# Optimization experiments

Hardware: AMD Instinct MI355X
Metric: run time of the kernel (lower is better)

The kernel has to match this reference:

```python
import jax, jax.numpy as jnp
import numpy as np

N_NODES = 100000


def setup_inputs() -> dict:
    key = jax.random.key(0)
    k1, k2, k3, k4, k5 = jax.random.split(key, 5)
    d_in, d_out, n_edges = 128, 128, 640000
    x = jax.random.normal(k1, (N_NODES, d_in), dtype=jnp.float32)
    edge_index = jax.random.randint(k2, (2, n_edges), 0, N_NODES, dtype=jnp.int64)
    # uniform(size, W) in the source is U(-1/sqrt(in), 1/sqrt(in)); scaled normal is fine as data
    s = 1.0 / np.sqrt(d_in)
    Wc = jax.random.normal(k3, (d_in, d_out), dtype=jnp.float32) * s
    Wn = jax.random.normal(k4, (d_in, d_out), dtype=jnp.float32) * s
    b = jax.random.normal(k5, (d_out,), dtype=jnp.float32) * s
    return {"x": x, "edge_index": edge_index, "Wc": Wc, "Wn": Wn, "b": b}


def reference(x, edge_index, Wc, Wn, b):
    row, col = edge_index[0], edge_index[1]
    alpha = x @ Wc                      # [N, out]
    beta = x @ Wn                       # [N, out]
    # Vectorized scatter-mean replacing the original per-node Python loop:
    # gamma[n] = mean(beta[col[row == n]])
    num = jax.ops.segment_sum(beta[col], row, num_segments=N_NODES)   # [N, out]
    cnt = jax.ops.segment_sum(jnp.ones_like(row, dtype=beta.dtype), row, num_segments=N_NODES)
    gamma = num / jnp.maximum(cnt, 1.0)[:, None]  # NOTE: unused below, exactly as in the original forward
    del gamma
    # The original returns alpha + beta + bias (gamma is dead code in the source).
    return alpha + beta + b
```

## Files before the change

### kernel.cpp

```cpp
#include <hip/hip_runtime.h>
#include <hip/hip_bf16.h>


#define NROWS 100000

typedef __attribute__((ext_vector_type(8))) __bf16 bf16x8;
typedef __attribute__((ext_vector_type(8))) unsigned short u16x8;
typedef __attribute__((ext_vector_type(4))) float f32x4;

__device__ __forceinline__ unsigned short f2bf(float f) {
    unsigned int u = __builtin_bit_cast(unsigned int, f);
    u += 0x7FFFu + ((u >> 16) & 1u);
    return (unsigned short)(u >> 16);
}

__device__ __forceinline__ bf16x8 pack8(const float4 lo, const float4 hi) {
    u16x8 r;
    r[0] = f2bf(lo.x); r[1] = f2bf(lo.y); r[2] = f2bf(lo.z); r[3] = f2bf(lo.w);
    r[4] = f2bf(hi.x); r[5] = f2bf(hi.y); r[6] = f2bf(hi.z); r[7] = f2bf(hi.w);
    return __builtin_bit_cast(bf16x8, r);
}

__global__ void prep_wt(const float* __restrict__ Wc, const float* __restrict__ Wn,
                        unsigned short* __restrict__ wt) {
    int i = blockIdx.x * 256 + threadIdx.x;
    int n = i >> 7, k = i & 127;
    wt[i] = f2bf(Wc[k * 128 + n] + Wn[k * 128 + n]);
}

__global__ __launch_bounds__(256) void gemm_bias(
    const float* __restrict__ x, const unsigned short* __restrict__ wt,
    const float* __restrict__ bias_g, float* __restrict__ out) {

    __shared__ __align__(16) unsigned short sWt[128 * 136];

    const int tid = threadIdx.x;
    #pragma unroll
    for (int it = 0; it < 8; ++it) {
        int idx8 = it * 256 + tid;
        int n = idx8 >> 4;
        int k = (idx8 & 15) << 3;
        *(u16x8*)&sWt[n * 136 + k] = *(const u16x8*)(wt + (idx8 << 3));
    }
    __syncthreads();

    const int wave = tid >> 6;
    const int lane = tid & 63;
    const int quad = lane >> 4;
    const int l16  = lane & 15;

    const long rowbase = (long)blockIdx.x * 128 + wave * 32;
    if (rowbase >= NROWS) return;

    float bv[8];
    #pragma unroll
    for (int ct = 0; ct < 8; ++ct) bv[ct] = bias_g[ct * 16 + l16];

    f32x4 acc[2][8] = {};

    const float* xr0 = x + (rowbase + l16) * 128;
    const float* xr1 = xr0 + 16 * 128;

    #pragma unroll
    for (int kc = 0; kc < 4; ++kc) {
        const int ko = kc * 32 + quad * 8;
        float4 a0lo = *(const float4*)(xr0 + ko);
        float4 a0hi = *(const float4*)(xr0 + ko + 4);
        float4 a1lo = *(const float4*)(xr1 + ko);
        float4 a1hi = *(const float4*)(xr1 + ko + 4);
        bf16x8 a0 = pack8(a0lo, a0hi);
        bf16x8 a1 = pack8(a1lo, a1hi);
        #pragma unroll
        for (int ct = 0; ct < 8; ++ct) {
            bf16x8 bf = *(const bf16x8*)&sWt[(ct * 16 + l16) * 136 + ko];
            acc[0][ct] = __builtin_amdgcn_mfma_f32_16x16x32_bf16(a0, bf, acc[0][ct], 0, 0, 0);
            acc[1][ct] = __builtin_amdgcn_mfma_f32_16x16x32_bf16(a1, bf, acc[1][ct], 0, 0, 0);
        }
    }

    #pragma unroll
    for (int mt = 0; mt < 2; ++mt) {
        #pragma unroll
        for (int r = 0; r < 4; ++r) {
            float* orow = out + (rowbase + mt * 16 + quad * 4 + r) * 128;
            #pragma unroll
            for (int ct = 0; ct < 8; ++ct) {
                orow[ct * 16 + l16] = acc[mt][ct][r] + bv[ct];
            }
        }
    }
}

extern "C" void kernel_launch(void* const* d_in, const int* in_sizes, int n_in,
                              void* d_out, int out_size, void* d_ws, size_t ws_size,
                              hipStream_t stream) {
    const float* x  = (const float*)d_in[0];
    const float* Wc = (const float*)d_in[2];
    const float* Wn = (const float*)d_in[3];
    const float* b  = (const float*)d_in[4];
    unsigned short* wt = (unsigned short*)d_ws;
    float* out = (float*)d_out;

    prep_wt<<<64, 256, 0, stream>>>(Wc, Wn, wt);
    const int nblocks = (NROWS + 127) / 128;
    gemm_bias<<<nblocks, 256, 0, stream>>>(x, wt, b, out);
}
```

Before: 112.9 us.

## Swap MFMA operands so each lane stores contiguous float4 outputs nontemporally

Swaps the A/B operands of the bf16 MFMA so the accumulator holds four consecutive output columns per lane instead of four rows. The epilogue can then write 16-byte vector stores with nontemporal hints instead of scalar 4-byte stores, and the bias is loaded as float4. It also replaces the manual round-to-nearest bf16 conversion with native __bf16 casts, which may lower to hardware convert instructions. The output is mathematically the same; the risk is small rounding-mode differences in the conversion.

```diff
diff --git a/kernel.cpp b/kernel.cpp
--- a/kernel.cpp
+++ b/kernel.cpp
@@ -8,31 +8,25 @@
 typedef __attribute__((ext_vector_type(8))) unsigned short u16x8;
 typedef __attribute__((ext_vector_type(4))) float f32x4;
 
-__device__ __forceinline__ unsigned short f2bf(float f) {
-    unsigned int u = __builtin_bit_cast(unsigned int, f);
-    u += 0x7FFFu + ((u >> 16) & 1u);
-    return (unsigned short)(u >> 16);
-}
-
 __device__ __forceinline__ bf16x8 pack8(const float4 lo, const float4 hi) {
-    u16x8 r;
-    r[0] = f2bf(lo.x); r[1] = f2bf(lo.y); r[2] = f2bf(lo.z); r[3] = f2bf(lo.w);
-    r[4] = f2bf(hi.x); r[5] = f2bf(hi.y); r[6] = f2bf(hi.z); r[7] = f2bf(hi.w);
-    return __builtin_bit_cast(bf16x8, r);
+    bf16x8 r;
+    r[0] = (__bf16)lo.x; r[1] = (__bf16)lo.y; r[2] = (__bf16)lo.z; r[3] = (__bf16)lo.w;
+    r[4] = (__bf16)hi.x; r[5] = (__bf16)hi.y; r[6] = (__bf16)hi.z; r[7] = (__bf16)hi.w;
+    return r;
 }
 
 __global__ void prep_wt(const float* __restrict__ Wc, const float* __restrict__ Wn,
-                        unsigned short* __restrict__ wt) {
+                        __bf16* __restrict__ wt) {
     int i = blockIdx.x * 256 + threadIdx.x;
     int n = i >> 7, k = i & 127;
-    wt[i] = f2bf(Wc[k * 128 + n] + Wn[k * 128 + n]);
+    wt[i] = (__bf16)(Wc[k * 128 + n] + Wn[k * 128 + n]);
 }
 
 __global__ __launch_bounds__(256) void gemm_bias(
-    const float* __restrict__ x, const unsigned short* __restrict__ wt,
+    const float* __restrict__ x, const __bf16* __restrict__ wt,
     const float* __restrict__ bias_g, float* __restrict__ out) {
 
-    __shared__ __align__(16) unsigned short sWt[128 * 136];
+    __shared__ __align__(16) __bf16 sWt[128 * 136];
 
     const int tid = threadIdx.x;
     #pragma unroll
@@ -40,7 +34,7 @@
         int idx8 = it * 256 + tid;
         int n = idx8 >> 4;
         int k = (idx8 & 15) << 3;
-        *(u16x8*)&sWt[n * 136 + k] = *(const u16x8*)(wt + (idx8 << 3));
+        *(bf16x8*)&sWt[n * 136 + k] = *(const bf16x8*)(wt + (idx8 << 3));
     }
     __syncthreads();
 
@@ -52,9 +46,10 @@
     const long rowbase = (long)blockIdx.x * 128 + wave * 32;
     if (rowbase >= NROWS) return;
 
-    float bv[8];
+    f32x4 bv[8];
     #pragma unroll
-    for (int ct = 0; ct < 8; ++ct) bv[ct] = bias_g[ct * 16 + l16];
+    for (int ct = 0; ct < 8; ++ct)
+        bv[ct] = *(const f32x4*)(bias_g + ct * 16 + quad * 4);
 
     f32x4 acc[2][8] = {};
 
@@ -64,29 +59,27 @@
     #pragma unroll
     for (int kc = 0; kc < 4; ++kc) {
         const int ko = kc * 32 + quad * 8;
-        float4 a0lo = *(const float4*)(xr0 + ko);
-        float4 a0hi = *(const float4*)(xr0 + ko + 4);
-        float4 a1lo = *(const float4*)(xr1 + ko);
-        float4 a1hi = *(const float4*)(xr1 + ko + 4);
-        bf16x8 a0 = pack8(a0lo, a0hi);
-        bf16x8 a1 = pack8(a1lo, a1hi);
+        float4 b0lo = *(const float4*)(xr0 + ko);
+        float4 b0hi = *(const float4*)(xr0 + ko + 4);
+        float4 b1lo = *(const float4*)(xr1 + ko);
+        float4 b1hi = *(const float4*)(xr1 + ko + 4);
+        bf16x8 xb0 = pack8(b0lo, b0hi);
+        bf16x8 xb1 = pack8(b1lo, b1hi);
         #pragma unroll
         for (int ct = 0; ct < 8; ++ct) {
-            bf16x8 bf = *(const bf16x8*)&sWt[(ct * 16 + l16) * 136 + ko];
-            acc[0][ct] = __builtin_amdgcn_mfma_f32_16x16x32_bf16(a0, bf, acc[0][ct], 0, 0, 0);
-            acc[1][ct] = __builtin_amdgcn_mfma_f32_16x16x32_bf16(a1, bf, acc[1][ct], 0, 0, 0);
+            bf16x8 wa = *(const bf16x8*)&sWt[(ct * 16 + l16) * 136 + ko];
+            acc[0][ct] = __builtin_amdgcn_mfma_f32_16x16x32_bf16(wa, xb0, acc[0][ct], 0, 0, 0);
+            acc[1][ct] = __builtin_amdgcn_mfma_f32_16x16x32_bf16(wa, xb1, acc[1][ct], 0, 0, 0);
         }
     }
 
     #pragma unroll
-    for (int mt = 0; mt < 2; ++mt) {
+    for (int g = 0; g < 2; ++g) {
+        float* orow = out + (rowbase + g * 16 + l16) * 128 + quad * 4;
         #pragma unroll
-        for (int r = 0; r < 4; ++r) {
-            float* orow = out + (rowbase + mt * 16 + quad * 4 + r) * 128;
-            #pragma unroll
-            for (int ct = 0; ct < 8; ++ct) {
-                orow[ct * 16 + l16] = acc[mt][ct][r] + bv[ct];
-            }
+        for (int ct = 0; ct < 8; ++ct) {
+            f32x4 v = acc[g][ct] + bv[ct];
+            __builtin_nontemporal_store(v, (f32x4*)(orow + ct * 16));
         }
     }
 }
@@ -98,7 +91,7 @@
     const float* Wc = (const float*)d_in[2];
     const float* Wn = (const float*)d_in[3];
     const float* b  = (const float*)d_in[4];
-    unsigned short* wt = (unsigned short*)d_ws;
+    __bf16* wt = (__bf16*)d_ws;
     float* out = (float*)d_out;
 
     prep_wt<<<64, 256, 0, stream>>>(Wc, Wn, wt);
```

New measurement: 116.7 us. 3.4% more time.
